# Kernel optimization log

Hardware: AMD Instinct MI355X
Metric: run time of the kernel (lower is better)

Reference implementation:

```python
import jax, jax.numpy as jnp
import numpy as np
from jax import lax

B, CIN, COUT, H, W = 4, 192, 192, 256, 256
K, S, P = 3, 1, 1


def setup_inputs() -> dict:
    key = jax.random.key(0)
    k1, k2, k3, k4 = jax.random.split(key, 4)
    x = jax.random.normal(k1, (B, CIN, H, W), dtype=jnp.float32)
    mask = jax.random.randint(k2, (B, 1, H, W), 0, 2, dtype=jnp.int32)
    fan_in = CIN * K * K
    bound = 1.0 / np.sqrt(fan_in)
    weight = jax.random.uniform(k3, (COUT, CIN, K, K), dtype=jnp.float32, minval=-bound, maxval=bound)
    bias = jax.random.uniform(k4, (COUT,), dtype=jnp.float32, minval=-bound, maxval=bound)
    return {"x": x, "mask": mask, "weight": weight, "bias": bias}


def reference(x, mask, weight, bias):
    # Dense conv (NCHW, OIHW). Equivalent to the unfold + matmul on gathered
    # patches; the custom scatter kernel writes results only at output
    # positions whose receptive field overlaps a nonzero mask entry,
    # leaving other positions zero.
    out = lax.conv_general_dilated(
        x, weight,
        window_strides=(S, S),
        padding=[(P, P), (P, P)],
        dimension_numbers=("NCHW", "OIHW", "NCHW"),
    ) + bias[None, :, None, None]

    # valid[b, 0, oh, ow] = any(mask patch != 0)  -> max-pool of (mask != 0)
    m = jnp.any(mask != 0, axis=1, keepdims=True).astype(out.dtype)  # [B,1,H,W]
    pooled = lax.reduce_window(
        m, 0.0, lax.max,
        window_dimensions=(1, 1, K, K),
        window_strides=(1, 1, S, S),
        padding=[(0, 0), (0, 0), (P, P), (P, P)],
    )  # [B,1,Hout,Wout]
    valid = (pooled > 0).astype(out.dtype)
    return out * valid
```

## Files before the change

kernel.cpp:

```cpp
#include <hip/hip_runtime.h>

typedef short short8 __attribute__((ext_vector_type(8)));
typedef __bf16 bf16x8 __attribute__((ext_vector_type(8)));
typedef float f32x4 __attribute__((ext_vector_type(4)));

#define HP 258

__device__ __forceinline__ short f2bf(float f) {
  unsigned u = __builtin_bit_cast(unsigned, f);
  unsigned r = u + 0x7fffu + ((u >> 16) & 1u);
  return (short)(r >> 16);
}

__device__ __forceinline__ void async16(void* l, const void* g) {
  __builtin_amdgcn_global_load_lds((const __attribute__((address_space(1))) void*)g,
                                   (__attribute__((address_space(3))) void*)l,
                                   16, 0, 0);
}

__global__ __launch_bounds__(256) void prepass(const float* __restrict__ x,
                                               const int* __restrict__ mask,
                                               const float* __restrict__ Wsrc,
                                               short* __restrict__ Xp,
                                               short* __restrict__ Wr,
                                               float* __restrict__ Vg) {
  __shared__ short lds[64 * 200];
  const int t = threadIdx.x;
  const int bid = blockIdx.x;

  if (bid < 4096) {
    const int w = t & 63;
    const int g = t >> 6;
    const int w0 = (bid & 3) << 6;
    const int ih = (bid >> 2) & 255;
    const int b = bid >> 10;
    const float* xb = x + ((size_t)b * 192) * 65536 + (size_t)ih * 256 + w0;
#pragma unroll
    for (int pass = 0; pass < 6; ++pass) {
      int ci = pass * 32 + g * 8;
      short8 v;
#pragma unroll
      for (int j = 0; j < 8; ++j) v[j] = f2bf(xb[(size_t)(ci + j) * 65536 + w]);
      *(short8*)&lds[w * 200 + ci] = v;
    }
    __syncthreads();
    short* dst = Xp + (((size_t)b * HP + (ih + 1)) * HP + (w0 + 1)) * 192;
#pragma unroll
    for (int i = 0; i < 6; ++i) {
      int gid = i * 256 + t;
      int ww = gid / 24;
      int c = gid - ww * 24;
      short8 vv = *(const short8*)&lds[ww * 200 + c * 8];
      *(short8*)&dst[(size_t)ww * 192 + c * 8] = vv;
    }
    return;
  }

  int rb = bid - 4096;
  if (rb < 386) {
    int gid = rb * 256 + t;
    if (gid >= 4 * 1028 * 24) return;
    int g = gid % 24;
    int pix = gid / 24;
    int b = pix / 1028;
    int i = pix - b * 1028;
    int h, w;
    if (i < 258)      { h = 0;   w = i; }
    else if (i < 516) { h = 257; w = i - 258; }
    else { int j = i - 516; h = 1 + (j >> 1); w = (j & 1) ? 257 : 0; }
    short8 z = {0, 0, 0, 0, 0, 0, 0, 0};
    *(short8*)&Xp[(((size_t)b * HP + h) * HP + w) * 192 + g * 8] = z;
    return;
  }
  rb -= 386;
  if (rb < 162) {
    int gid = rb * 256 + t;
    if (gid >= 9 * 6 * 768) return;
    int gr = gid % 768;
    int tk = gid / 768;
    int kc = tk % 6;
    int tap = tk / 6;
    int co = gr >> 2;
    int q = (gr & 3) ^ (co & 3);
    int ci = kc * 32 + q * 8;
    short8 v;
#pragma unroll
    for (int j = 0; j < 8; ++j) v[j] = f2bf(Wsrc[(size_t)(co * 192 + ci + j) * 9 + tap]);
    *(short8*)&Wr[(size_t)gid * 8] = v;
    return;
  }
  rb -= 162;
  {
    int gid = rb * 256 + t;
    int b = gid >> 16;
    int r = gid & 65535;
    int oh = r >> 8;
    int ow = r & 255;
    const int* mb = mask + ((size_t)b << 16);
    int any = 0;
    for (int dh = -1; dh <= 1; ++dh) {
      int h = oh + dh;
      if ((unsigned)h >= 256u) continue;
      for (int dw = -1; dw <= 1; ++dw) {
        int w = ow + dw;
        if ((unsigned)w >= 256u) continue;
        any |= (mb[h * 256 + w] != 0);
      }
    }
    Vg[gid] = any ? 1.0f : 0.0f;
  }
}

__global__ __launch_bounds__(256) void conv_mfma(
    const short* __restrict__ Xp,
    const short* __restrict__ Wr,
    const float* __restrict__ Vg,
    const float* __restrict__ bias,
    float* __restrict__ out)
{
  __shared__ short Al[2][768 * 8];
  __shared__ short Bl[2][512 * 8];

  const int t = threadIdx.x;
  const int lane = t & 63;
  const int wave = t >> 6;
  const int quad = lane >> 4;
  const int l16 = lane & 15;

  const int b = blockIdx.z;
  const int by = blockIdx.y;
  const int oh = ((by & 3) << 6) | (by >> 2);
  const int ow0 = blockIdx.x << 7;

  const int axor = quad ^ (l16 & 3);
  int aoff[3];
#pragma unroll
  for (int c = 0; c < 3; ++c) aoff[c] = ((wave * 48 + c * 16 + l16) * 4 + axor) * 8;
  int boff[8];
#pragma unroll
  for (int s = 0; s < 8; ++s) boff[s] = ((s * 16 + l16) * 4 + axor) * 8;

  const int p0 = t >> 2;
  const int q0 = (t & 3) ^ (p0 & 3);
  const int poff = p0 * 192 + q0 * 8;

  const f32x4 fzero = {0.f, 0.f, 0.f, 0.f};
  f32x4 acc[3][8];
#pragma unroll
  for (int c = 0; c < 3; ++c)
#pragma unroll
    for (int s = 0; s < 8; ++s) acc[c][s] = fzero;

  const short* wbase = Wr + (size_t)t * 8;
  const short* xbase = Xp + (size_t)b * HP * HP * 192 + ((size_t)oh * HP + ow0) * 192 + poff;

  async16(&Al[0][t * 8], wbase);
  async16(&Al[0][(t + 256) * 8], wbase + 256 * 8);
  async16(&Al[0][(t + 512) * 8], wbase + 512 * 8);
  async16(&Bl[0][t * 8], xbase);
  async16(&Bl[0][(t + 256) * 8], xbase + 64 * 192);
  __syncthreads();

#pragma unroll
  for (int s = 0; s < 54; ++s) {
    const int cb = s & 1;
    const int sn = s + 1;
    if (sn < 54) {
      const int tap = sn / 6;
      const int kc = sn - tap * 6;
      const int kh = tap / 3;
      const int kw = tap - kh * 3;
      const short* wsrc = wbase + (size_t)sn * (768 * 8);
      async16(&Al[cb ^ 1][t * 8], wsrc);
      async16(&Al[cb ^ 1][(t + 256) * 8], wsrc + 256 * 8);
      async16(&Al[cb ^ 1][(t + 512) * 8], wsrc + 512 * 8);
      const short* xsrc = xbase + ((size_t)kh * HP + kw) * 192 + kc * 32;
      async16(&Bl[cb ^ 1][t * 8], xsrc);
      async16(&Bl[cb ^ 1][(t + 256) * 8], xsrc + 64 * 192);
    }
    short8 a[3], bb[8];
#pragma unroll
    for (int c = 0; c < 3; ++c) a[c] = *(const short8*)&Al[cb][aoff[c]];
#pragma unroll
    for (int k = 0; k < 8; ++k) bb[k] = *(const short8*)&Bl[cb][boff[k]];
    __builtin_amdgcn_s_setprio(1);
#pragma unroll
    for (int c = 0; c < 3; ++c)
#pragma unroll
      for (int k = 0; k < 8; ++k)
        acc[c][k] = __builtin_amdgcn_mfma_f32_16x16x32_bf16(
            __builtin_bit_cast(bf16x8, a[c]), __builtin_bit_cast(bf16x8, bb[k]),
            acc[c][k], 0, 0, 0);
    __builtin_amdgcn_s_setprio(0);
    __syncthreads();
  }

  float bv[3][4];
#pragma unroll
  for (int c = 0; c < 3; ++c)
#pragma unroll
    for (int r = 0; r < 4; ++r) bv[c][r] = bias[wave * 48 + c * 16 + quad * 4 + r];

  const float* vrow = Vg + ((size_t)b * 256 + oh) * 256 + ow0;
  float* ob = out + (size_t)(b * 192) * 65536 + (size_t)oh * 256 + ow0;
#pragma unroll
  for (int s = 0; s < 8; ++s) {
    float v = vrow[s * 16 + l16];
#pragma unroll
    for (int c = 0; c < 3; ++c) {
      int cobase = wave * 48 + c * 16 + quad * 4;
#pragma unroll
      for (int r = 0; r < 4; ++r)
        ob[(size_t)(cobase + r) * 65536 + s * 16 + l16] = (acc[c][s][r] + bv[c][r]) * v;
    }
  }
}

__global__ __launch_bounds__(256) void naive_conv(
    const float* __restrict__ x, const int* __restrict__ mask,
    const float* __restrict__ w, const float* __restrict__ bias,
    float* __restrict__ out) {
  size_t gid = (size_t)blockIdx.x * 256 + threadIdx.x;
  int ow = (int)(gid & 255);
  int oh = (int)((gid >> 8) & 255);
  int rest = (int)(gid >> 16);
  int co = rest % 192;
  int b = rest / 192;
  int any = 0;
  for (int dh = -1; dh <= 1; ++dh) {
    int h = oh + dh;
    if ((unsigned)h >= 256u) continue;
    for (int dw = -1; dw <= 1; ++dw) {
      int ww2 = ow + dw;
      if ((unsigned)ww2 >= 256u) continue;
      any |= (mask[((size_t)b << 16) + h * 256 + ww2] != 0);
    }
  }
  if (!any) { out[gid] = 0.f; return; }
  float acc = bias[co];
  const float* xb = x + (size_t)b * 192 * 65536;
  const float* wc = w + (size_t)co * 192 * 9;
  for (int ci = 0; ci < 192; ++ci) {
    const float* xc = xb + (size_t)ci * 65536;
    const float* wk = wc + ci * 9;
    for (int kh = 0; kh < 3; ++kh) {
      int h = oh + kh - 1;
      if ((unsigned)h >= 256u) continue;
      for (int kw = 0; kw < 3; ++kw) {
        int w2 = ow + kw - 1;
        if ((unsigned)w2 >= 256u) continue;
        acc += xc[h * 256 + w2] * wk[kh * 3 + kw];
      }
    }
  }
  out[gid] = acc;
}

extern "C" void kernel_launch(void* const* d_in, const int* in_sizes, int n_in,
                              void* d_out, int out_size, void* d_ws, size_t ws_size,
                              hipStream_t stream) {
  const float* x = (const float*)d_in[0];
  const int* mask = (const int*)d_in[1];
  const float* w = (const float*)d_in[2];
  const float* bias = (const float*)d_in[3];
  float* out = (float*)d_out;

  const size_t xp_bytes = (size_t)4 * HP * HP * 192 * 2;
  const size_t wr_bytes = (size_t)9 * 6 * 768 * 8 * 2;
  const size_t vg_bytes = (size_t)4 * 256 * 256 * 4;

  if (d_ws && ws_size >= xp_bytes + wr_bytes + vg_bytes) {
    short* Xp = (short*)d_ws;
    short* Wr = (short*)((char*)d_ws + xp_bytes);
    float* Vg = (float*)((char*)d_ws + xp_bytes + wr_bytes);
    prepass<<<5668, 256, 0, stream>>>(x, mask, w, Xp, Wr, Vg);
    conv_mfma<<<dim3(2, 256, 4), 256, 0, stream>>>(Xp, Wr, Vg, bias, out);
  } else {
    naive_conv<<<196608, 256, 0, stream>>>(x, mask, w, bias, out);
  }
}
```

Measured before the change: 541.4 us.

## Process two K-chunks per pipeline stage and change LDS swizzle pattern

After: 494.4 us. 1.1x faster.

```diff
diff --git a/kernel.cpp b/kernel.cpp
--- a/kernel.cpp
+++ b/kernel.cpp
@@ -81,7 +81,7 @@
     int kc = tk % 6;
     int tap = tk / 6;
     int co = gr >> 2;
-    int q = (gr & 3) ^ (co & 3);
+    int q = (gr & 3) ^ ((co >> 1) & 3);
     int ci = kc * 32 + q * 8;
     short8 v;
 #pragma unroll
@@ -118,8 +118,8 @@
     const float* __restrict__ bias,
     float* __restrict__ out)
 {
-  __shared__ short Al[2][768 * 8];
-  __shared__ short Bl[2][512 * 8];
+  __shared__ short Al[2][2][768 * 8];
+  __shared__ short Bl[2][2][512 * 8];
 
   const int t = threadIdx.x;
   const int lane = t & 63;
@@ -132,7 +132,7 @@
   const int oh = ((by & 3) << 6) | (by >> 2);
   const int ow0 = blockIdx.x << 7;
 
-  const int axor = quad ^ (l16 & 3);
+  const int axor = quad ^ ((l16 >> 1) & 3);
   int aoff[3];
 #pragma unroll
   for (int c = 0; c < 3; ++c) aoff[c] = ((wave * 48 + c * 16 + l16) * 4 + axor) * 8;
@@ -141,7 +141,7 @@
   for (int s = 0; s < 8; ++s) boff[s] = ((s * 16 + l16) * 4 + axor) * 8;
 
   const int p0 = t >> 2;
-  const int q0 = (t & 3) ^ (p0 & 3);
+  const int q0 = (t & 3) ^ ((p0 >> 1) & 3);
   const int poff = p0 * 192 + q0 * 8;
 
   const f32x4 fzero = {0.f, 0.f, 0.f, 0.f};
@@ -154,44 +154,54 @@
   const short* wbase = Wr + (size_t)t * 8;
   const short* xbase = Xp + (size_t)b * HP * HP * 192 + ((size_t)oh * HP + ow0) * 192 + poff;
 
-  async16(&Al[0][t * 8], wbase);
-  async16(&Al[0][(t + 256) * 8], wbase + 256 * 8);
-  async16(&Al[0][(t + 512) * 8], wbase + 512 * 8);
-  async16(&Bl[0][t * 8], xbase);
-  async16(&Bl[0][(t + 256) * 8], xbase + 64 * 192);
+  auto stageA = [&](int buf, const short* wsrc) {
+    async16(&Al[buf][0][t * 8], wsrc);
+    async16(&Al[buf][0][(t + 256) * 8], wsrc + 2048);
+    async16(&Al[buf][0][(t + 512) * 8], wsrc + 4096);
+    async16(&Al[buf][1][t * 8], wsrc + 6144);
+    async16(&Al[buf][1][(t + 256) * 8], wsrc + 6144 + 2048);
+    async16(&Al[buf][1][(t + 512) * 8], wsrc + 6144 + 4096);
+  };
+  auto stageB = [&](int buf, const short* xsrc) {
+    async16(&Bl[buf][0][t * 8], xsrc);
+    async16(&Bl[buf][0][(t + 256) * 8], xsrc + 64 * 192);
+    async16(&Bl[buf][1][t * 8], xsrc + 32);
+    async16(&Bl[buf][1][(t + 256) * 8], xsrc + 64 * 192 + 32);
+  };
+
+  stageA(0, wbase);
+  stageB(0, xbase);
   __syncthreads();
 
 #pragma unroll
-  for (int s = 0; s < 54; ++s) {
+  for (int s = 0; s < 27; ++s) {
     const int cb = s & 1;
     const int sn = s + 1;
-    if (sn < 54) {
-      const int tap = sn / 6;
-      const int kc = sn - tap * 6;
+    if (sn < 27) {
+      const int tap = sn / 3;
+      const int kcp = sn - tap * 3;
       const int kh = tap / 3;
       const int kw = tap - kh * 3;
-      const short* wsrc = wbase + (size_t)sn * (768 * 8);
-      async16(&Al[cb ^ 1][t * 8], wsrc);
-      async16(&Al[cb ^ 1][(t + 256) * 8], wsrc + 256 * 8);
-      async16(&Al[cb ^ 1][(t + 512) * 8], wsrc + 512 * 8);
-      const short* xsrc = xbase + ((size_t)kh * HP + kw) * 192 + kc * 32;
-      async16(&Bl[cb ^ 1][t * 8], xsrc);
-      async16(&Bl[cb ^ 1][(t + 256) * 8], xsrc + 64 * 192);
-    }
-    short8 a[3], bb[8];
-#pragma unroll
-    for (int c = 0; c < 3; ++c) a[c] = *(const short8*)&Al[cb][aoff[c]];
-#pragma unroll
-    for (int k = 0; k < 8; ++k) bb[k] = *(const short8*)&Bl[cb][boff[k]];
-    __builtin_amdgcn_s_setprio(1);
-#pragma unroll
-    for (int c = 0; c < 3; ++c)
-#pragma unroll
-      for (int k = 0; k < 8; ++k)
-        acc[c][k] = __builtin_amdgcn_mfma_f32_16x16x32_bf16(
-            __builtin_bit_cast(bf16x8, a[c]), __builtin_bit_cast(bf16x8, bb[k]),
-            acc[c][k], 0, 0, 0);
-    __builtin_amdgcn_s_setprio(0);
+      stageA(cb ^ 1, wbase + (size_t)(tap * 6 + kcp * 2) * 6144);
+      stageB(cb ^ 1, xbase + ((size_t)kh * HP + kw) * 192 + kcp * 64);
+    }
+#pragma unroll
+    for (int h = 0; h < 2; ++h) {
+      short8 a[3], bb[8];
+#pragma unroll
+      for (int c = 0; c < 3; ++c) a[c] = *(const short8*)&Al[cb][h][aoff[c]];
+#pragma unroll
+      for (int k = 0; k < 8; ++k) bb[k] = *(const short8*)&Bl[cb][h][boff[k]];
+      __builtin_amdgcn_s_setprio(1);
+#pragma unroll
+      for (int c = 0; c < 3; ++c)
+#pragma unroll
+        for (int k = 0; k < 8; ++k)
+          acc[c][k] = __builtin_amdgcn_mfma_f32_16x16x32_bf16(
+              __builtin_bit_cast(bf16x8, a[c]), __builtin_bit_cast(bf16x8, bb[k]),
+              acc[c][k], 0, 0, 0);
+      __builtin_amdgcn_s_setprio(0);
+    }
     __syncthreads();
   }
 
```
